# Performance work log

Hardware: AMD Instinct MI355X
Metric: run time of the kernel (lower is better)

Reference implementation:

```python
import jax, jax.numpy as jnp
import numpy as np

B, S, D, H = 128, 512, 256, 256


def _lstm_cell(Wih, Whh, b, x_t, h, c):
    # PyTorch LSTM gate order: i, f, g, o. b = b_ih + b_hh (mathematically equivalent).
    z = x_t @ Wih.T + h @ Whh.T + b  # [B, 4H]
    i, f, g, o = jnp.split(z, 4, axis=-1)
    i = jax.nn.sigmoid(i)
    f = jax.nn.sigmoid(f)
    g = jnp.tanh(g)
    o = jax.nn.sigmoid(o)
    c = f * c + i * g
    h = o * jnp.tanh(c)
    return h, c


def setup_inputs() -> dict:
    key = jax.random.key(0)
    ks = jax.random.split(key, 12)
    s = 1.0 / np.sqrt(H)
    f32 = jnp.float32
    return {
        "x": jax.random.normal(ks[0], (B, S, D), f32),
        "enc_Wih": jax.random.uniform(ks[1], (4 * H, D), f32, -s, s),
        "enc_Whh": jax.random.uniform(ks[2], (4 * H, H), f32, -s, s),
        "enc_b": jax.random.uniform(ks[3], (4 * H,), f32, -s, s),
        "dec_Wih": jax.random.uniform(ks[4], (4 * H, D), f32, -s, s),
        "dec_Whh": jax.random.uniform(ks[5], (4 * H, H), f32, -s, s),
        "dec_b": jax.random.uniform(ks[6], (4 * H,), f32, -s, s),
        "W1_w": jax.random.uniform(ks[7], (H, H), f32, -s, s),
        "W1_b": jax.random.uniform(ks[8], (H,), f32, -s, s),
        "W2_w": jax.random.uniform(ks[9], (H, H), f32, -s, s),
        "W2_b": jax.random.uniform(ks[10], (H,), f32, -s, s),
        "vt_w": jax.random.uniform(ks[11], (H,), f32, -s, s),
    }


def reference(x, enc_Wih, enc_Whh, enc_b, dec_Wih, dec_Whh, dec_b,
              W1_w, W1_b, W2_w, W2_b, vt_w):
    b_, s_, d_ = x.shape
    h0 = jnp.zeros((b_, H), x.dtype)
    c0 = jnp.zeros((b_, H), x.dtype)

    # ---- encoder LSTM over time ----
    def enc_step(carry, x_t):
        h, c = carry
        h, c = _lstm_cell(enc_Wih, enc_Whh, enc_b, x_t, h, c)
        return (h, c), h

    (h, c), enc_out = jax.lax.scan(enc_step, (h0, c0), jnp.swapaxes(x, 0, 1))
    enc_out = jnp.swapaxes(enc_out, 0, 1)  # [B, S, H]

    # W1(encoder_outputs) is loop-invariant; compute once (same math as original)
    enc_proj = enc_out @ W1_w.T + W1_b  # [B, S, H]

    # ---- pointer decode loop ----
    def dec_step(carry, _):
        h, c, din = carry
        h, c = _lstm_cell(dec_Wih, dec_Whh, dec_b, din, h, c)
        q = h @ W2_w.T + W2_b  # [B, H]
        u = jnp.einsum('bsh,h->bs', jnp.tanh(enc_proj + q[:, None, :]), vt_w)
        probs = jax.nn.softmax(u, axis=1)  # [B, S]
        din = jnp.einsum('bs,bsh->bh', probs, enc_out)
        return (h, c, din), probs

    din0 = jnp.zeros((b_, d_), x.dtype)
    _, probs_seq = jax.lax.scan(dec_step, (h, c, din0), None, length=s_)
    return jnp.swapaxes(probs_seq, 0, 1)  # [B, S, S]
```

## Files before the change

### kernel.cpp

```cpp
#include <hip/hip_runtime.h>
#include <hip/hip_fp16.h>

typedef _Float16 h2_t __attribute__((ext_vector_type(2)));
typedef unsigned int u32x4 __attribute__((ext_vector_type(4)));

#define KEXP 2.8853900817779268f

#define BARRIER() do { \
    asm volatile("s_waitcnt lgkmcnt(0)" ::: "memory"); \
    __builtin_amdgcn_s_barrier(); \
    asm volatile("" ::: "memory"); \
} while (0)

__device__ __forceinline__ float fdot2(unsigned int a, unsigned int b, float c) {
#if __has_builtin(__builtin_amdgcn_fdot2)
    return __builtin_amdgcn_fdot2(__builtin_bit_cast(h2_t, a), __builtin_bit_cast(h2_t, b), c, false);
#else
    h2_t ha = __builtin_bit_cast(h2_t, a), hb = __builtin_bit_cast(h2_t, b);
    return c + (float)ha[0]*(float)hb[0] + (float)ha[1]*(float)hb[1];
#endif
}

__device__ __forceinline__ unsigned int pk16(float a, float b) {
    auto h = __builtin_amdgcn_cvt_pkrtz(a, b);
    return __builtin_bit_cast(unsigned int, h);
}

__device__ __forceinline__ float rcp_(float x) {
#if __has_builtin(__builtin_amdgcn_rcpf)
    return __builtin_amdgcn_rcpf(x);
#else
    return 1.0f / x;
#endif
}

__device__ __forceinline__ float sigm(float x) { return rcp_(1.0f + __expf(-x)); }
__device__ __forceinline__ float tanh_(float x) {
    float e = __expf(2.0f * x);
    return 1.0f - 2.0f * rcp_(e + 1.0f);
}

__device__ __forceinline__ unsigned int rcp1p2exp(unsigned int s) {
    __half2 e = h2exp2(__builtin_bit_cast(__half2, s));
    __half2 d = __hadd2(e, __float2half2_rn(1.0f));
    return __builtin_bit_cast(unsigned int, h2rcp(d));
}
__device__ __forceinline__ unsigned int hadd2u(unsigned int a, unsigned int b) {
    return __builtin_bit_cast(unsigned int,
        __hadd2(__builtin_bit_cast(__half2, a), __builtin_bit_cast(__half2, b)));
}

__device__ __forceinline__ void st_u32(unsigned int* p, unsigned int v) {
    __hip_atomic_store(p, v, __ATOMIC_RELAXED, __HIP_MEMORY_SCOPE_AGENT);
}
__device__ __forceinline__ unsigned int ld_u32(const unsigned int* p) {
    return __hip_atomic_load(p, __ATOMIC_RELAXED, __HIP_MEMORY_SCOPE_AGENT);
}
__device__ __forceinline__ float h2f_lo(unsigned int v) {
    return __half2float(__ushort_as_half((unsigned short)(v & 0xffffu)));
}
__device__ __forceinline__ float h2f_hi(unsigned int v) {
    return __half2float(__ushort_as_half((unsigned short)(v >> 16)));
}

__global__ void init_flags_kernel(unsigned int* flags) {
    flags[threadIdx.x * 32] = 0u;
}

__global__ __launch_bounds__(256) void prep_kernel(
    const float* __restrict__ encWhh, const float* __restrict__ decWih,
    const float* __restrict__ decWhh, const float* __restrict__ W2w,
    u32x4* __restrict__ We8, u32x4* __restrict__ Wi8, u32x4* __restrict__ Wh8, u32x4* __restrict__ W28)
{
    int id = blockIdx.x * 256 + threadIdx.x;
    if (id < 3 * 32768) {
        int mat = id >> 15, local = id & 32767;
        int j = local & 1023, k8 = local >> 10;
        const float* src = mat == 0 ? encWhh : (mat == 1 ? decWih : decWhh);
        u32x4* dst = mat == 0 ? We8 : (mat == 1 ? Wi8 : Wh8);
        const float* p = src + (size_t)j * 256 + k8 * 8;
        float4 a = *(const float4*)p; float4 c = *(const float4*)(p + 4);
        u32x4 v; v[0] = pk16(a.x, a.y); v[1] = pk16(a.z, a.w);
        v[2] = pk16(c.x, c.y); v[3] = pk16(c.z, c.w);
        dst[k8 * 1024 + j] = v;
    } else {
        int local = id - 3 * 32768;
        if (local < 8192) {
            int m = local & 255, k8 = local >> 8;
            const float* p = W2w + (size_t)m * 256 + k8 * 8;
            float4 a = *(const float4*)p; float4 c = *(const float4*)(p + 4);
            u32x4 v; v[0] = pk16(a.x, a.y); v[1] = pk16(a.z, a.w);
            v[2] = pk16(c.x, c.y); v[3] = pk16(c.z, c.w);
            W28[k8 * 256 + m] = v;
        }
    }
}

template<int A_IS_F16, int TR_OUT>
__global__ __launch_bounds__(256) void gemm_kernel(
    const void* __restrict__ A_, const float* __restrict__ Bw,
    const float* __restrict__ bias, unsigned short* __restrict__ C, int N, float scale)
{
    __shared__ float As[16][68];
    __shared__ float Bs[16][132];
    const int t = threadIdx.x;
    const int row0 = blockIdx.y * 64, col0 = blockIdx.x * 128;
    const int ty = t >> 4, tx = t & 15;
    const int lm = t & 63, lkq = t >> 6;
    const int ln = t & 127, lkq2 = t >> 7;
    float acc[4][8] = {};
    for (int k0 = 0; k0 < 256; k0 += 16) {
        float4 av;
        if constexpr (A_IS_F16) {
            const unsigned short* A = (const unsigned short*)A_;
            uint2 ha = *(const uint2*)(A + (size_t)(row0 + lm) * 256 + k0 + lkq * 4);
            h2_t h0 = __builtin_bit_cast(h2_t, ha.x);
            h2_t h1 = __builtin_bit_cast(h2_t, ha.y);
            av = make_float4((float)h0[0], (float)h0[1], (float)h1[0], (float)h1[1]);
        } else {
            av = *(const float4*)((const float*)A_ + (size_t)(row0 + lm) * 256 + k0 + lkq * 4);
        }
        const float* bp = Bw + (size_t)(col0 + ln) * 256 + k0 + lkq2 * 8;
        float4 bv0 = *(const float4*)bp;
        float4 bv1 = *(const float4*)(bp + 4);
        __syncthreads();
        As[lkq * 4 + 0][lm] = av.x;
        As[lkq * 4 + 1][lm] = av.y;
        As[lkq * 4 + 2][lm] = av.z;
        As[lkq * 4 + 3][lm] = av.w;
        Bs[lkq2 * 8 + 0][ln] = bv0.x;
        Bs[lkq2 * 8 + 1][ln] = bv0.y;
        Bs[lkq2 * 8 + 2][ln] = bv0.z;
        Bs[lkq2 * 8 + 3][ln] = bv0.w;
        Bs[lkq2 * 8 + 4][ln] = bv1.x;
        Bs[lkq2 * 8 + 5][ln] = bv1.y;
        Bs[lkq2 * 8 + 6][ln] = bv1.z;
        Bs[lkq2 * 8 + 7][ln] = bv1.w;
        __syncthreads();
        #pragma unroll
        for (int kk = 0; kk < 16; ++kk) {
            float4 a = *(float4*)&As[kk][ty * 4];
            float4 b0 = *(float4*)&Bs[kk][tx * 8];
            float4 b1 = *(float4*)&Bs[kk][tx * 8 + 4];
            float ar[4] = {a.x, a.y, a.z, a.w};
            float br[8] = {b0.x, b0.y, b0.z, b0.w, b1.x, b1.y, b1.z, b1.w};
            #pragma unroll
            for (int i = 0; i < 4; ++i)
                #pragma unroll
                for (int j = 0; j < 8; ++j)
                    acc[i][j] = fmaf(ar[i], br[j], acc[i][j]);
        }
    }
    float bv[8];
    #pragma unroll
    for (int j = 0; j < 8; ++j) bv[j] = bias[col0 + tx * 8 + j];
    #pragma unroll
    for (int i = 0; i < 4; ++i) {
        unsigned int w0 = pk16((acc[i][0] + bv[0]) * scale, (acc[i][1] + bv[1]) * scale);
        unsigned int w1 = pk16((acc[i][2] + bv[2]) * scale, (acc[i][3] + bv[3]) * scale);
        unsigned int w2 = pk16((acc[i][4] + bv[4]) * scale, (acc[i][5] + bv[5]) * scale);
        unsigned int w3 = pk16((acc[i][6] + bv[6]) * scale, (acc[i][7] + bv[7]) * scale);
        uint4 val = make_uint4(w0, w1, w2, w3);
        if constexpr (TR_OUT) {
            int rr = row0 + ty * 4 + i;
            int bb = rr >> 9, s = rr & 511;
            int c8 = (col0 >> 3) + tx;
            ((uint4*)C)[(size_t)bb * 16384 + (size_t)c8 * 512 + s] = val;
        } else {
            *(uint4*)(C + (size_t)(row0 + ty * 4 + i) * N + col0 + tx * 8) = val;
        }
    }
}

__global__ __launch_bounds__(1024) void encoder_kernel(
    const unsigned short* __restrict__ Xproj, const u32x4* __restrict__ We8,
    float* __restrict__ hfin, float* __restrict__ cfin,
    unsigned short* __restrict__ enc_h, unsigned int* __restrict__ encT)
{
    const int b = blockIdx.x, t = threadIdx.x;
    __shared__ __align__(16) float zs[1024];
    __shared__ __align__(16) unsigned int hh2[128];
    if (t < 128) hh2[t] = 0u;
    float c_reg = 0.f, hprev = 0.f, hcur = 0.f;
    __syncthreads();
    const unsigned short* xp = Xproj + (size_t)b * 512 * 1024 + t;
    for (int step = 0; step < 512; ++step) {
        float acc = __half2float(__ushort_as_half(__builtin_nontemporal_load(xp)));
        #pragma unroll 8
        for (int k8 = 0; k8 < 32; ++k8) {
            u32x4 wv = We8[k8 * 1024 + t];
            u32x4 hv = *(const u32x4*)&hh2[k8 * 4];
            acc = fdot2(wv[0], hv[0], acc); acc = fdot2(wv[1], hv[1], acc);
            acc = fdot2(wv[2], hv[2], acc); acc = fdot2(wv[3], hv[3], acc);
        }
        zs[t] = acc;
        __syncthreads();
        if (t < 256) {
            float ig = sigm(zs[t]), fg = sigm(zs[t + 256]);
            float gg = tanh_(zs[t + 512]), og = sigm(zs[t + 768]);
            c_reg = fg * c_reg + ig * gg;
            float h = og * tanh_(c_reg);
            float hnb = __shfl_down(h, 1);
            if (!(t & 1)) hh2[t >> 1] = pk16(h, hnb);
            __builtin_nontemporal_store(__half_as_ushort(__float2half_rn(h)),
                                        enc_h + (size_t)(b * 512 + step) * 256 + t);
            if (step & 1) {
                int s2 = step >> 1;
                encT[(size_t)b * 65536 + (size_t)((s2 >> 2) * 256 + t) * 4 + (s2 & 3)] = pk16(hprev, h);
            }
            hprev = h; hcur = h;
        }
        __syncthreads();
        xp += 1024;
    }
    if (t < 256) { hfin[b * 256 + t] = hcur; cfin[b * 256 + t] = c_reg; }
}

__global__ __launch_bounds__(512, 4) void decoder_kernel(
    const u32x4* __restrict__ Wi8, const u32x4* __restrict__ Wh8, const u32x4* __restrict__ W28,
    const float* __restrict__ dec_b, const float* __restrict__ W2b, const float* __restrict__ vtw,
    const float* __restrict__ hfin, const float* __restrict__ cfin,
    const u32x4* __restrict__ projT, const u32x4* __restrict__ encT,
    unsigned int* __restrict__ xgate, unsigned int* __restrict__ xdin,
    unsigned int* __restrict__ xsum, unsigned int* __restrict__ flags,
    float* __restrict__ out)
{
    const int blk = blockIdx.x;
    const int b = blk & 127, g = blk >> 7;
    const int t = threadIdx.x;
    const int lane = t & 63, w = t >> 6;

    __shared__ __align__(16) float zs[512];
    __shared__ __align__(16) unsigned int hh2[128];
    __shared__ __align__(16) unsigned int din2[128];
    __shared__ __align__(16) unsigned int qp2[128];
    __shared__ __align__(16) unsigned int mv2u[128];
    __shared__ __align__(16) unsigned int p2u[64];
    __shared__ float wreds[8];
    __shared__ float svtS, rsS;

    const int q4 = b * 4 + g;
    unsigned int* fl_me = flags + q4 * 32;
    unsigned int* fl_p0 = flags + (b * 4 + ((g + 1) & 3)) * 32;
    unsigned int* fl_p1 = flags + (b * 4 + ((g + 2) & 3)) * 32;
    unsigned int* fl_p2 = flags + (b * 4 + ((g + 3) & 3)) * 32;
    unsigned int* xg_me = xgate + q4 * 128;
    unsigned int* xd_me = xdin + q4 * 256;

    float ca = 0.f, cb = 0.f;
    if (t < 128) {
        ca = cfin[b * 256 + 2 * t];
        cb = cfin[b * 256 + 2 * t + 1];
        din2[t] = 0u;
        mv2u[t] = pk16(-2.f * vtw[2 * t], -2.f * vtw[2 * t + 1]);
    }
    const float bja = (t < 256) ? dec_b[g * 256 + t] : 0.f;
    const float w2b_r = (t < 256) ? W2b[t] : 0.f;
    if (t < 256) zs[t] = vtw[t];
    __syncthreads();
    if (t < 64) {
        float v = zs[t] + zs[t + 64] + zs[t + 128] + zs[t + 192];
        #pragma unroll
        for (int off = 1; off < 64; off <<= 1) v += __shfl_xor(v, off);
        if (t == 0) svtS = v;
    }
    if (t < 256) {
        float h0 = hfin[b * 256 + t];
        float hnb = __shfl_down(h0, 1);
        if (!(t & 1)) hh2[t >> 1] = pk16(h0, hnb);
    }
    __syncthreads();
    const float svt = svtS;

    const int jl = t & 255, kh = t >> 8;
    const u32x4* wp = (kh ? Wh8 : Wi8) + (g * 256 + jl);
    const unsigned int* vls = kh ? (const unsigned int*)hh2 : (const unsigned int*)din2;
    const int mC = t & 255, sc = t >> 8;
    const int sl4 = t >> 2, qr = t & 3;
    const int s_g = g * 128 + sl4;
    const u32x4* pD = projT + (size_t)b * 16384 + (size_t)(qr * 8) * 512 + s_g;
    const u32x4* fD = encT + (size_t)b * 16384 + (size_t)(g * 16 + sc * 8) * 256 + mC;
    float* outp = out + (size_t)b * 262144;

    for (int step = 0; step < 512; ++step) {
        float acc = 0.f;
        #pragma unroll 8
        for (int k8 = 0; k8 < 32; ++k8) {
            u32x4 wv = wp[k8 * 1024];
            u32x4 hv = *(const u32x4*)&vls[k8 * 4];
            acc = fdot2(wv[0], hv[0], acc); acc = fdot2(wv[1], hv[1], acc);
            acc = fdot2(wv[2], hv[2], acc); acc = fdot2(wv[3], hv[3], acc);
        }
        zs[t] = acc;
        BARRIER();
        if (t < 256) {
            float z = bja + zs[t] + zs[t + 256];
            float gv = (g == 2) ? tanh_(z) : sigm(z);
            float gnx = __shfl_down(gv, 1);
            if (!(t & 1))
                st_u32(&xg_me[t >> 1],
                       (unsigned int)__half_as_ushort(__float2half_rn(gv)) |
                       ((unsigned int)__half_as_ushort(__float2half_rn(gnx)) << 16));
        }
        asm volatile("s_waitcnt vmcnt(0)" ::: "memory");
        BARRIER();
        if (t == 0) {
            unsigned int T = (unsigned)(2 * step + 1);
            st_u32(fl_me, T);
            for (;;) {
                unsigned int f0 = ld_u32(fl_p0), f1 = ld_u32(fl_p1), f2 = ld_u32(fl_p2);
                if (f0 >= T && f1 >= T && f2 >= T) break;
                __builtin_amdgcn_s_sleep(1);
            }
        }
        BARRIER();
        if (t < 128) {
            unsigned int G0 = ld_u32(&xgate[(b * 4 + 0) * 128 + t]);
            unsigned int G1 = ld_u32(&xgate[(b * 4 + 1) * 128 + t]);
            unsigned int G2 = ld_u32(&xgate[(b * 4 + 2) * 128 + t]);
            unsigned int G3 = ld_u32(&xgate[(b * 4 + 3) * 128 + t]);
            ca = h2f_lo(G1) * ca + h2f_lo(G0) * h2f_lo(G2);
            cb = h2f_hi(G1) * cb + h2f_hi(G0) * h2f_hi(G2);
            float ha = h2f_lo(G3) * tanh_(ca);
            float hb = h2f_hi(G3) * tanh_(cb);
            hh2[t] = pk16(ha, hb);
        }
        BARRIER();
        {
            float qa = 0.f;
            #pragma unroll
            for (int i = 0; i < 16; ++i) {
                int k8 = sc * 16 + i;
                u32x4 wv = W28[k8 * 256 + mC];
                u32x4 hv = *(const u32x4*)&hh2[k8 * 4];
                qa = fdot2(wv[0], hv[0], qa); qa = fdot2(wv[1], hv[1], qa);
                qa = fdot2(wv[2], hv[2], qa); qa = fdot2(wv[3], hv[3], qa);
            }
            zs[t] = qa;
        }
        BARRIER();
        if (t < 256) {
            float q = (w2b_r + zs[t] + zs[t + 256]) * KEXP;
            float qnx = __shfl_down(q, 1);
            if (!(t & 1)) qp2[t >> 1] = pk16(q, qnx);
        }
        BARRIER();
        float e;
        u32x4 fv[8];
        {
            float up = 0.f;
            #pragma unroll 4
            for (int i = 0; i < 8; ++i) {
                u32x4 pv = pD[i * 512];
                int c = qr * 8 + i;
                u32x4 qh = *(const u32x4*)&qp2[c * 4];
                u32x4 mv = *(const u32x4*)&mv2u[c * 4];
                up = fdot2(mv[0], rcp1p2exp(hadd2u(pv[0], qh[0])), up);
                up = fdot2(mv[1], rcp1p2exp(hadd2u(pv[1], qh[1])), up);
                up = fdot2(mv[2], rcp1p2exp(hadd2u(pv[2], qh[2])), up);
                up = fdot2(mv[3], rcp1p2exp(hadd2u(pv[3], qh[3])), up);
            }
            up += __shfl_xor(up, 1);
            up += __shfl_xor(up, 2);
            e = __expf(up + svt);
            #pragma unroll
            for (int j = 0; j < 8; ++j) fv[j] = fD[j * 256];
            float enx = __shfl_down(e, 4);
            if (!(t & 7)) p2u[t >> 3] = pk16(e, enx);
            float ws = e;
            #pragma unroll
            for (int off = 1; off < 64; off <<= 1) ws += __shfl_xor(ws, off);
            if (lane == 0) wreds[w] = ws;
        }
        BARRIER();
        {
            float fa = 0.f;
            #pragma unroll
            for (int j = 0; j < 8; ++j) {
                u32x4 ev = fv[j];
                u32x4 pw = *(const u32x4*)&p2u[(sc * 8 + j) * 4];
                fa = fdot2(ev[0], pw[0], fa); fa = fdot2(ev[1], pw[1], fa);
                fa = fdot2(ev[2], pw[2], fa); fa = fdot2(ev[3], pw[3], fa);
            }
            zs[t] = fa;
        }
        BARRIER();
        float dpart = 0.f;
        if (t < 256) {
            dpart = zs[t] + zs[t + 256];
            st_u32(&xd_me[t], __builtin_bit_cast(unsigned int, dpart));
        }
        if (t == 0) {
            float ls = 0.f;
            #pragma unroll
            for (int k = 0; k < 8; ++k) ls += wreds[k];
            st_u32(&xsum[q4 * 32], __builtin_bit_cast(unsigned int, ls * 0.25f));
        }
        asm volatile("s_waitcnt vmcnt(0)" ::: "memory");
        BARRIER();
        if (t == 0) {
            unsigned int T = (unsigned)(2 * step + 2);
            st_u32(fl_me, T);
            for (;;) {
                unsigned int f0 = ld_u32(fl_p0), f1 = ld_u32(fl_p1), f2 = ld_u32(fl_p2);
                if (f0 >= T && f1 >= T && f2 >= T) break;
                __builtin_amdgcn_s_sleep(1);
            }
            float gs = __builtin_bit_cast(float, ld_u32(&xsum[(b * 4 + 0) * 32]))
                     + __builtin_bit_cast(float, ld_u32(&xsum[(b * 4 + 1) * 32]))
                     + __builtin_bit_cast(float, ld_u32(&xsum[(b * 4 + 2) * 32]))
                     + __builtin_bit_cast(float, ld_u32(&xsum[(b * 4 + 3) * 32]));
            rsS = rcp_(gs);
        }
        BARRIER();
        {
            float rs = rsS;
            if (t < 256) {
                float dsum = dpart;
                #pragma unroll
                for (int dg = 1; dg < 4; ++dg) {
                    int gp = (g + dg) & 3;
                    dsum += __builtin_bit_cast(float, ld_u32(&xdin[(b * 4 + gp) * 256 + t]));
                }
                float dval = dsum * rs;
                float dnx = __shfl_down(dval, 1);
                if (!(t & 1)) din2[t >> 1] = pk16(dval, dnx);
            }
            if ((t & 3) == 0)
                outp[(size_t)step * 512 + s_g] = e * rs;
        }
        BARRIER();
    }
}

extern "C" void kernel_launch(void* const* d_in, const int* in_sizes, int n_in,
                              void* d_out, int out_size, void* d_ws, size_t ws_size,
                              hipStream_t stream) {
    const float* x      = (const float*)d_in[0];
    const float* encWih = (const float*)d_in[1];
    const float* encWhh = (const float*)d_in[2];
    const float* enc_b  = (const float*)d_in[3];
    const float* decWih = (const float*)d_in[4];
    const float* decWhh = (const float*)d_in[5];
    const float* dec_bp = (const float*)d_in[6];
    const float* W1w    = (const float*)d_in[7];
    const float* W1b    = (const float*)d_in[8];
    const float* W2w    = (const float*)d_in[9];
    const float* W2bp   = (const float*)d_in[10];
    const float* vtw    = (const float*)d_in[11];

    char* ws = (char*)d_ws;
    u32x4* We8 = (u32x4*)(ws);
    u32x4* Wi8 = (u32x4*)(ws + 524288);
    u32x4* Wh8 = (u32x4*)(ws + 1048576);
    u32x4* W28 = (u32x4*)(ws + 1572864);
    unsigned short* enc_h = (unsigned short*)(ws + 1703936);
    unsigned int*   encT  = (unsigned int*)(ws + 35258368);
    unsigned short* projT = (unsigned short*)(ws + 68812800);
    float* hfin = (float*)(ws + 102367232);
    float* cfin = (float*)(ws + 102498304);

    unsigned int* flags = (unsigned int*)(ws + 1703936);
    unsigned int* xsum  = (unsigned int*)(ws + 1703936 + 65536);
    unsigned int* xgate = (unsigned int*)(ws + 1703936 + 131072);
    unsigned int* xdin  = (unsigned int*)(ws + 1703936 + 131072 + 262144);

    unsigned short* Xproj = (unsigned short*)d_out;

    prep_kernel<<<416, 256, 0, stream>>>(encWhh, decWih, decWhh, W2w, We8, Wi8, Wh8, W28);
    gemm_kernel<0, 0><<<dim3(8, 1024), 256, 0, stream>>>(x, encWih, enc_b, Xproj, 1024, 1.0f);
    encoder_kernel<<<128, 1024, 0, stream>>>(Xproj, We8, hfin, cfin, enc_h, (unsigned int*)encT);
    gemm_kernel<1, 1><<<dim3(2, 1024), 256, 0, stream>>>(enc_h, W1w, W1b, projT, 256, KEXP);
    init_flags_kernel<<<1, 512, 0, stream>>>(flags);
    decoder_kernel<<<512, 512, 0, stream>>>(Wi8, Wh8, W28, dec_bp, W2bp, vtw,
                                            hfin, cfin, (const u32x4*)projT, (const u32x4*)encT,
                                            xgate, xdin, xsum, flags, (float*)d_out);
}
```

Measured before the change: 16.86 ms.

## Batch four sequences per decoder block with register-resident LSTM weights

The decoder now processes four batch elements per workgroup (128 blocks instead of 512). Each thread keeps its slice of the input and recurrent LSTM weights in registers for the whole run, so these weights are no longer re-read from memory every step, and one weight fetch serves four dot products. The cost is much higher register pressure (launch bounds drop to 2 waves/EU), fewer blocks to spread across CUs, and four times more serial per-block work in the attention and softmax phases. Cross-block flag synchronization is now shared by four batches at once.

```diff
diff --git a/kernel.cpp b/kernel.cpp
--- a/kernel.cpp
+++ b/kernel.cpp
@@ -21,6 +21,12 @@
 #endif
 }
 
+__device__ __forceinline__ float dot4(u32x4 a, u32x4 b, float c) {
+    c = fdot2(a[0], b[0], c); c = fdot2(a[1], b[1], c);
+    c = fdot2(a[2], b[2], c); c = fdot2(a[3], b[3], c);
+    return c;
+}
+
 __device__ __forceinline__ unsigned int pk16(float a, float b) {
     auto h = __builtin_amdgcn_cvt_pkrtz(a, b);
     return __builtin_bit_cast(unsigned int, h);
@@ -55,6 +61,9 @@
 }
 __device__ __forceinline__ unsigned int ld_u32(const unsigned int* p) {
     return __hip_atomic_load(p, __ATOMIC_RELAXED, __HIP_MEMORY_SCOPE_AGENT);
+}
+__device__ __forceinline__ float ld_f32(const unsigned int* p) {
+    return __builtin_bit_cast(float, ld_u32(p));
 }
 __device__ __forceinline__ float h2f_lo(unsigned int v) {
     return __half2float(__ushort_as_half((unsigned short)(v & 0xffffu)));
@@ -190,8 +199,7 @@
         for (int k8 = 0; k8 < 32; ++k8) {
             u32x4 wv = We8[k8 * 1024 + t];
             u32x4 hv = *(const u32x4*)&hh2[k8 * 4];
-            acc = fdot2(wv[0], hv[0], acc); acc = fdot2(wv[1], hv[1], acc);
-            acc = fdot2(wv[2], hv[2], acc); acc = fdot2(wv[3], hv[3], acc);
+            acc = dot4(wv, hv, acc);
         }
         zs[t] = acc;
         __syncthreads();
@@ -216,7 +224,7 @@
     if (t < 256) { hfin[b * 256 + t] = hcur; cfin[b * 256 + t] = c_reg; }
 }
 
-__global__ __launch_bounds__(512, 4) void decoder_kernel(
+__global__ __launch_bounds__(512, 2) void decoder_kernel(
     const u32x4* __restrict__ Wi8, const u32x4* __restrict__ Wh8, const u32x4* __restrict__ W28,
     const float* __restrict__ dec_b, const float* __restrict__ W2b, const float* __restrict__ vtw,
     const float* __restrict__ hfin, const float* __restrict__ cfin,
@@ -226,81 +234,108 @@
     float* __restrict__ out)
 {
     const int blk = blockIdx.x;
-    const int b = blk & 127, g = blk >> 7;
+    const int gr = blk & 31, g = blk >> 5;
     const int t = threadIdx.x;
     const int lane = t & 63, w = t >> 6;
-
-    __shared__ __align__(16) float zs[512];
-    __shared__ __align__(16) unsigned int hh2[128];
-    __shared__ __align__(16) unsigned int din2[128];
-    __shared__ __align__(16) unsigned int qp2[128];
+    const int bbase = gr * 4;
+
+    __shared__ float zsp[4][512];
+    __shared__ __align__(16) unsigned int hh2[4][128];
+    __shared__ __align__(16) unsigned int din2[4][128];
+    __shared__ __align__(16) unsigned int qp2[4][128];
     __shared__ __align__(16) unsigned int mv2u[128];
-    __shared__ __align__(16) unsigned int p2u[64];
-    __shared__ float wreds[8];
-    __shared__ float svtS, rsS;
-
-    const int q4 = b * 4 + g;
-    unsigned int* fl_me = flags + q4 * 32;
-    unsigned int* fl_p0 = flags + (b * 4 + ((g + 1) & 3)) * 32;
-    unsigned int* fl_p1 = flags + (b * 4 + ((g + 2) & 3)) * 32;
-    unsigned int* fl_p2 = flags + (b * 4 + ((g + 3) & 3)) * 32;
-    unsigned int* xg_me = xgate + q4 * 128;
-    unsigned int* xd_me = xdin + q4 * 256;
-
-    float ca = 0.f, cb = 0.f;
+    __shared__ __align__(16) unsigned int p2u[4][64];
+    __shared__ float wreds[8][4];
+    __shared__ float svtS, rsS[4];
+
+    const int r = t & 255, kh = t >> 8;
+    u32x4 wih[16], whh[16];
+    #pragma unroll
+    for (int i = 0; i < 16; ++i) wih[i] = Wi8[(size_t)(kh * 16 + i) * 1024 + g * 256 + r];
+    #pragma unroll
+    for (int i = 0; i < 16; ++i) whh[i] = Wh8[(size_t)(kh * 16 + i) * 1024 + g * 256 + r];
+
+    float cA[4], cB[4];
+    #pragma unroll
+    for (int b = 0; b < 4; ++b) { cA[b] = 0.f; cB[b] = 0.f; }
     if (t < 128) {
-        ca = cfin[b * 256 + 2 * t];
-        cb = cfin[b * 256 + 2 * t + 1];
-        din2[t] = 0u;
+        #pragma unroll
+        for (int b = 0; b < 4; ++b) {
+            cA[b] = cfin[(bbase + b) * 256 + 2 * t];
+            cB[b] = cfin[(bbase + b) * 256 + 2 * t + 1];
+            din2[b][t] = 0u;
+        }
         mv2u[t] = pk16(-2.f * vtw[2 * t], -2.f * vtw[2 * t + 1]);
     }
     const float bja = (t < 256) ? dec_b[g * 256 + t] : 0.f;
     const float w2b_r = (t < 256) ? W2b[t] : 0.f;
-    if (t < 256) zs[t] = vtw[t];
+    if (t < 256) zsp[0][t] = vtw[t];
     __syncthreads();
     if (t < 64) {
-        float v = zs[t] + zs[t + 64] + zs[t + 128] + zs[t + 192];
+        float v = zsp[0][t] + zsp[0][t + 64] + zsp[0][t + 128] + zsp[0][t + 192];
         #pragma unroll
         for (int off = 1; off < 64; off <<= 1) v += __shfl_xor(v, off);
         if (t == 0) svtS = v;
     }
     if (t < 256) {
-        float h0 = hfin[b * 256 + t];
-        float hnb = __shfl_down(h0, 1);
-        if (!(t & 1)) hh2[t >> 1] = pk16(h0, hnb);
+        #pragma unroll
+        for (int b = 0; b < 4; ++b) {
+            float h0 = hfin[(bbase + b) * 256 + t];
+            float h0n = __shfl_down(h0, 1);
+            if (!(t & 1)) hh2[b][t >> 1] = pk16(h0, h0n);
+        }
     }
     __syncthreads();
     const float svt = svtS;
 
-    const int jl = t & 255, kh = t >> 8;
-    const u32x4* wp = (kh ? Wh8 : Wi8) + (g * 256 + jl);
-    const unsigned int* vls = kh ? (const unsigned int*)hh2 : (const unsigned int*)din2;
-    const int mC = t & 255, sc = t >> 8;
-    const int sl4 = t >> 2, qr = t & 3;
-    const int s_g = g * 128 + sl4;
-    const u32x4* pD = projT + (size_t)b * 16384 + (size_t)(qr * 8) * 512 + s_g;
-    const u32x4* fD = encT + (size_t)b * 16384 + (size_t)(g * 16 + sc * 8) * 256 + mC;
-    float* outp = out + (size_t)b * 262144;
+    const int q4 = gr * 4 + g;
+    unsigned int* fl_me = flags + q4 * 32;
+    unsigned int* fl_p0 = flags + (gr * 4 + ((g + 1) & 3)) * 32;
+    unsigned int* fl_p1 = flags + (gr * 4 + ((g + 2) & 3)) * 32;
+    unsigned int* fl_p2 = flags + (gr * 4 + ((g + 3) & 3)) * 32;
+    unsigned int* xg_me = xgate + q4 * 512;
+    unsigned int* xd_me = xdin + q4 * 1024;
+
+    const int sl = t >> 2, qr = t & 3;
+    const int hF = t & 255, scF = t >> 8;
+    const size_t pDoff = (size_t)(qr * 8) * 512 + g * 128 + sl;
+    const size_t fDoff = (size_t)(g * 16 + scF * 8) * 256 + hF;
 
     for (int step = 0; step < 512; ++step) {
-        float acc = 0.f;
-        #pragma unroll 8
-        for (int k8 = 0; k8 < 32; ++k8) {
-            u32x4 wv = wp[k8 * 1024];
-            u32x4 hv = *(const u32x4*)&vls[k8 * 4];
-            acc = fdot2(wv[0], hv[0], acc); acc = fdot2(wv[1], hv[1], acc);
-            acc = fdot2(wv[2], hv[2], acc); acc = fdot2(wv[3], hv[3], acc);
-        }
-        zs[t] = acc;
+        {
+            float a0 = 0.f, a1 = 0.f, a2 = 0.f, a3 = 0.f;
+            #pragma unroll
+            for (int i = 0; i < 16; ++i) {
+                u32x4 wv = wih[i];
+                u32x4 d0 = *(const u32x4*)&din2[0][kh * 64 + i * 4];
+                u32x4 d1 = *(const u32x4*)&din2[1][kh * 64 + i * 4];
+                u32x4 d2 = *(const u32x4*)&din2[2][kh * 64 + i * 4];
+                u32x4 d3 = *(const u32x4*)&din2[3][kh * 64 + i * 4];
+                a0 = dot4(wv, d0, a0); a1 = dot4(wv, d1, a1);
+                a2 = dot4(wv, d2, a2); a3 = dot4(wv, d3, a3);
+            }
+            #pragma unroll
+            for (int i = 0; i < 16; ++i) {
+                u32x4 wv = whh[i];
+                u32x4 h0 = *(const u32x4*)&hh2[0][kh * 64 + i * 4];
+                u32x4 h1 = *(const u32x4*)&hh2[1][kh * 64 + i * 4];
+                u32x4 h2 = *(const u32x4*)&hh2[2][kh * 64 + i * 4];
+                u32x4 h3 = *(const u32x4*)&hh2[3][kh * 64 + i * 4];
+                a0 = dot4(wv, h0, a0); a1 = dot4(wv, h1, a1);
+                a2 = dot4(wv, h2, a2); a3 = dot4(wv, h3, a3);
+            }
+            zsp[0][t] = a0; zsp[1][t] = a1; zsp[2][t] = a2; zsp[3][t] = a3;
+        }
         BARRIER();
         if (t < 256) {
-            float z = bja + zs[t] + zs[t + 256];
-            float gv = (g == 2) ? tanh_(z) : sigm(z);
-            float gnx = __shfl_down(gv, 1);
-            if (!(t & 1))
-                st_u32(&xg_me[t >> 1],
-                       (unsigned int)__half_as_ushort(__float2half_rn(gv)) |
-                       ((unsigned int)__half_as_ushort(__float2half_rn(gnx)) << 16));
+            float gv[4];
+            #pragma unroll
+            for (int b = 0; b < 4; ++b) {
+                float z = bja + zsp[b][t] + zsp[b][t + 256];
+                gv[b] = (g == 2) ? tanh_(z) : sigm(z);
+            }
+            st_u32(&xg_me[t], pk16(gv[0], gv[1]));
+            st_u32(&xg_me[256 + t], pk16(gv[2], gv[3]));
         }
         asm volatile("s_waitcnt vmcnt(0)" ::: "memory");
         BARRIER();
@@ -315,86 +350,116 @@
         }
         BARRIER();
         if (t < 128) {
-            unsigned int G0 = ld_u32(&xgate[(b * 4 + 0) * 128 + t]);
-            unsigned int G1 = ld_u32(&xgate[(b * 4 + 1) * 128 + t]);
-            unsigned int G2 = ld_u32(&xgate[(b * 4 + 2) * 128 + t]);
-            unsigned int G3 = ld_u32(&xgate[(b * 4 + 3) * 128 + t]);
-            ca = h2f_lo(G1) * ca + h2f_lo(G0) * h2f_lo(G2);
-            cb = h2f_hi(G1) * cb + h2f_hi(G0) * h2f_hi(G2);
-            float ha = h2f_lo(G3) * tanh_(ca);
-            float hb = h2f_hi(G3) * tanh_(cb);
-            hh2[t] = pk16(ha, hb);
+            #pragma unroll
+            for (int bp = 0; bp < 2; ++bp) {
+                unsigned int Xi_a = ld_u32(&xgate[(gr * 4 + 0) * 512 + bp * 256 + 2 * t]);
+                unsigned int Xi_b = ld_u32(&xgate[(gr * 4 + 0) * 512 + bp * 256 + 2 * t + 1]);
+                unsigned int Xf_a = ld_u32(&xgate[(gr * 4 + 1) * 512 + bp * 256 + 2 * t]);
+                unsigned int Xf_b = ld_u32(&xgate[(gr * 4 + 1) * 512 + bp * 256 + 2 * t + 1]);
+                unsigned int Xg_a = ld_u32(&xgate[(gr * 4 + 2) * 512 + bp * 256 + 2 * t]);
+                unsigned int Xg_b = ld_u32(&xgate[(gr * 4 + 2) * 512 + bp * 256 + 2 * t + 1]);
+                unsigned int Xo_a = ld_u32(&xgate[(gr * 4 + 3) * 512 + bp * 256 + 2 * t]);
+                unsigned int Xo_b = ld_u32(&xgate[(gr * 4 + 3) * 512 + bp * 256 + 2 * t + 1]);
+                int b0i = bp * 2, b1i = bp * 2 + 1;
+                cA[b0i] = h2f_lo(Xf_a) * cA[b0i] + h2f_lo(Xi_a) * h2f_lo(Xg_a);
+                cB[b0i] = h2f_lo(Xf_b) * cB[b0i] + h2f_lo(Xi_b) * h2f_lo(Xg_b);
+                hh2[b0i][t] = pk16(h2f_lo(Xo_a) * tanh_(cA[b0i]), h2f_lo(Xo_b) * tanh_(cB[b0i]));
+                cA[b1i] = h2f_hi(Xf_a) * cA[b1i] + h2f_hi(Xi_a) * h2f_hi(Xg_a);
+                cB[b1i] = h2f_hi(Xf_b) * cB[b1i] + h2f_hi(Xi_b) * h2f_hi(Xg_b);
+                hh2[b1i][t] = pk16(h2f_hi(Xo_a) * tanh_(cA[b1i]), h2f_hi(Xo_b) * tanh_(cB[b1i]));
+            }
         }
         BARRIER();
         {
-            float qa = 0.f;
-            #pragma unroll
+            float q0 = 0.f, q1 = 0.f, q2 = 0.f, q3 = 0.f;
+            #pragma unroll 4
             for (int i = 0; i < 16; ++i) {
-                int k8 = sc * 16 + i;
-                u32x4 wv = W28[k8 * 256 + mC];
-                u32x4 hv = *(const u32x4*)&hh2[k8 * 4];
-                qa = fdot2(wv[0], hv[0], qa); qa = fdot2(wv[1], hv[1], qa);
-                qa = fdot2(wv[2], hv[2], qa); qa = fdot2(wv[3], hv[3], qa);
-            }
-            zs[t] = qa;
+                int k8 = kh * 16 + i;
+                u32x4 wv = W28[k8 * 256 + r];
+                u32x4 h0 = *(const u32x4*)&hh2[0][k8 * 4];
+                u32x4 h1 = *(const u32x4*)&hh2[1][k8 * 4];
+                u32x4 h2 = *(const u32x4*)&hh2[2][k8 * 4];
+                u32x4 h3 = *(const u32x4*)&hh2[3][k8 * 4];
+                q0 = dot4(wv, h0, q0); q1 = dot4(wv, h1, q1);
+                q2 = dot4(wv, h2, q2); q3 = dot4(wv, h3, q3);
+            }
+            zsp[0][t] = q0; zsp[1][t] = q1; zsp[2][t] = q2; zsp[3][t] = q3;
         }
         BARRIER();
         if (t < 256) {
-            float q = (w2b_r + zs[t] + zs[t + 256]) * KEXP;
-            float qnx = __shfl_down(q, 1);
-            if (!(t & 1)) qp2[t >> 1] = pk16(q, qnx);
-        }
-        BARRIER();
-        float e;
-        u32x4 fv[8];
+            #pragma unroll
+            for (int b = 0; b < 4; ++b) {
+                float q = (w2b_r + zsp[b][t] + zsp[b][t + 256]) * KEXP;
+                float qn = __shfl_down(q, 1);
+                if (!(t & 1)) qp2[b][t >> 1] = pk16(q, qn);
+            }
+        }
+        BARRIER();
+        float eb[4];
         {
-            float up = 0.f;
-            #pragma unroll 4
-            for (int i = 0; i < 8; ++i) {
-                u32x4 pv = pD[i * 512];
-                int c = qr * 8 + i;
-                u32x4 qh = *(const u32x4*)&qp2[c * 4];
-                u32x4 mv = *(const u32x4*)&mv2u[c * 4];
-                up = fdot2(mv[0], rcp1p2exp(hadd2u(pv[0], qh[0])), up);
-                up = fdot2(mv[1], rcp1p2exp(hadd2u(pv[1], qh[1])), up);
-                up = fdot2(mv[2], rcp1p2exp(hadd2u(pv[2], qh[2])), up);
-                up = fdot2(mv[3], rcp1p2exp(hadd2u(pv[3], qh[3])), up);
-            }
-            up += __shfl_xor(up, 1);
-            up += __shfl_xor(up, 2);
-            e = __expf(up + svt);
-            #pragma unroll
-            for (int j = 0; j < 8; ++j) fv[j] = fD[j * 256];
-            float enx = __shfl_down(e, 4);
-            if (!(t & 7)) p2u[t >> 3] = pk16(e, enx);
-            float ws = e;
-            #pragma unroll
-            for (int off = 1; off < 64; off <<= 1) ws += __shfl_xor(ws, off);
-            if (lane == 0) wreds[w] = ws;
+            #pragma unroll
+            for (int b = 0; b < 4; ++b) {
+                const u32x4* pD = projT + (size_t)(bbase + b) * 16384 + pDoff;
+                u32x4 pv[8];
+                #pragma unroll
+                for (int i = 0; i < 8; ++i) pv[i] = pD[i * 512];
+                float u = 0.f;
+                #pragma unroll
+                for (int i = 0; i < 8; ++i) {
+                    int c = qr * 8 + i;
+                    u32x4 qh = *(const u32x4*)&qp2[b][c * 4];
+                    u32x4 mv = *(const u32x4*)&mv2u[c * 4];
+                    u = fdot2(mv[0], rcp1p2exp(hadd2u(pv[i][0], qh[0])), u);
+                    u = fdot2(mv[1], rcp1p2exp(hadd2u(pv[i][1], qh[1])), u);
+                    u = fdot2(mv[2], rcp1p2exp(hadd2u(pv[i][2], qh[2])), u);
+                    u = fdot2(mv[3], rcp1p2exp(hadd2u(pv[i][3], qh[3])), u);
+                }
+                u += __shfl_xor(u, 1);
+                u += __shfl_xor(u, 2);
+                float e = __expf(u + svt);
+                eb[b] = e;
+                float en = __shfl_down(e, 4);
+                if (!(t & 7)) p2u[b][t >> 3] = pk16(e, en);
+                float ws = e;
+                #pragma unroll
+                for (int off = 1; off < 64; off <<= 1) ws += __shfl_xor(ws, off);
+                if (lane == 0) wreds[w][b] = ws;
+            }
         }
         BARRIER();
         {
-            float fa = 0.f;
-            #pragma unroll
-            for (int j = 0; j < 8; ++j) {
-                u32x4 ev = fv[j];
-                u32x4 pw = *(const u32x4*)&p2u[(sc * 8 + j) * 4];
-                fa = fdot2(ev[0], pw[0], fa); fa = fdot2(ev[1], pw[1], fa);
-                fa = fdot2(ev[2], pw[2], fa); fa = fdot2(ev[3], pw[3], fa);
-            }
-            zs[t] = fa;
-        }
-        BARRIER();
-        float dpart = 0.f;
+            #pragma unroll
+            for (int b = 0; b < 4; ++b) {
+                const u32x4* fD = encT + (size_t)(bbase + b) * 16384 + fDoff;
+                u32x4 fv[8];
+                #pragma unroll
+                for (int j = 0; j < 8; ++j) fv[j] = fD[j * 256];
+                float fa = 0.f;
+                #pragma unroll
+                for (int j = 0; j < 8; ++j) {
+                    u32x4 pw = *(const u32x4*)&p2u[b][(scF * 8 + j) * 4];
+                    fa = dot4(fv[j], pw, fa);
+                }
+                zsp[b][t] = fa;
+            }
+        }
+        BARRIER();
+        float dp[4] = {0.f, 0.f, 0.f, 0.f};
         if (t < 256) {
-            dpart = zs[t] + zs[t + 256];
-            st_u32(&xd_me[t], __builtin_bit_cast(unsigned int, dpart));
+            #pragma unroll
+            for (int b = 0; b < 4; ++b) {
+                dp[b] = zsp[b][t] + zsp[b][t + 256];
+                st_u32(&xd_me[b * 256 + t], __builtin_bit_cast(unsigned int, dp[b]));
+            }
         }
         if (t == 0) {
-            float ls = 0.f;
-            #pragma unroll
-            for (int k = 0; k < 8; ++k) ls += wreds[k];
-            st_u32(&xsum[q4 * 32], __builtin_bit_cast(unsigned int, ls * 0.25f));
+            #pragma unroll
+            for (int b = 0; b < 4; ++b) {
+                float s = 0.f;
+                #pragma unroll
+                for (int k = 0; k < 8; ++k) s += wreds[k][b];
+                st_u32(&xsum[q4 * 32 + b], __builtin_bit_cast(unsigned int, s * 0.25f));
+            }
         }
         asm volatile("s_waitcnt vmcnt(0)" ::: "memory");
         BARRIER();
@@ -406,28 +471,35 @@
                 if (f0 >= T && f1 >= T && f2 >= T) break;
                 __builtin_amdgcn_s_sleep(1);
             }
-            float gs = __builtin_bit_cast(float, ld_u32(&xsum[(b * 4 + 0) * 32]))
-                     + __builtin_bit_cast(float, ld_u32(&xsum[(b * 4 + 1) * 32]))
-                     + __builtin_bit_cast(float, ld_u32(&xsum[(b * 4 + 2) * 32]))
-                     + __builtin_bit_cast(float, ld_u32(&xsum[(b * 4 + 3) * 32]));
-            rsS = rcp_(gs);
+            #pragma unroll
+            for (int b = 0; b < 4; ++b) {
+                float gs = 0.f;
+                #pragma unroll
+                for (int gp = 0; gp < 4; ++gp) gs += ld_f32(&xsum[(gr * 4 + gp) * 32 + b]);
+                rsS[b] = rcp_(gs);
+            }
         }
         BARRIER();
         {
-            float rs = rsS;
             if (t < 256) {
-                float dsum = dpart;
-                #pragma unroll
-                for (int dg = 1; dg < 4; ++dg) {
-                    int gp = (g + dg) & 3;
-                    dsum += __builtin_bit_cast(float, ld_u32(&xdin[(b * 4 + gp) * 256 + t]));
+                #pragma unroll
+                for (int b = 0; b < 4; ++b) {
+                    float d = dp[b];
+                    #pragma unroll
+                    for (int dg = 1; dg < 4; ++dg) {
+                        int gp = (g + dg) & 3;
+                        d += ld_f32(&xdin[(gr * 4 + gp) * 1024 + b * 256 + t]);
+                    }
+                    float dv = d * rsS[b];
+                    float dvn = __shfl_down(dv, 1);
+                    if (!(t & 1)) din2[b][t >> 1] = pk16(dv, dvn);
                 }
-                float dval = dsum * rs;
-                float dnx = __shfl_down(dval, 1);
-                if (!(t & 1)) din2[t >> 1] = pk16(dval, dnx);
-            }
-            if ((t & 3) == 0)
-                outp[(size_t)step * 512 + s_g] = e * rs;
+            }
+            if (!(t & 3)) {
+                #pragma unroll
+                for (int b = 0; b < 4; ++b)
+                    out[(size_t)(bbase + b) * 262144 + (size_t)step * 512 + g * 128 + sl] = eb[b] * rsS[b];
+            }
         }
         BARRIER();
     }
@@ -461,9 +533,9 @@
     float* cfin = (float*)(ws + 102498304);
 
     unsigned int* flags = (unsigned int*)(ws + 1703936);
-    unsigned int* xsum  = (unsigned int*)(ws + 1703936 + 65536);
-    unsigned int* xgate = (unsigned int*)(ws + 1703936 + 131072);
-    unsigned int* xdin  = (unsigned int*)(ws + 1703936 + 131072 + 262144);
+    unsigned int* xsum  = (unsigned int*)(ws + 1703936 + 32768);
+    unsigned int* xgate = (unsigned int*)(ws + 1703936 + 65536);
+    unsigned int* xdin  = (unsigned int*)(ws + 1703936 + 65536 + 262144);
 
     unsigned short* Xproj = (unsigned short*)d_out;
 
@@ -471,8 +543,8 @@
     gemm_kernel<0, 0><<<dim3(8, 1024), 256, 0, stream>>>(x, encWih, enc_b, Xproj, 1024, 1.0f);
     encoder_kernel<<<128, 1024, 0, stream>>>(Xproj, We8, hfin, cfin, enc_h, (unsigned int*)encT);
     gemm_kernel<1, 1><<<dim3(2, 1024), 256, 0, stream>>>(enc_h, W1w, W1b, projT, 256, KEXP);
-    init_flags_kernel<<<1, 512, 0, stream>>>(flags);
-    decoder_kernel<<<512, 512, 0, stream>>>(Wi8, Wh8, W28, dec_bp, W2bp, vtw,
+    init_flags_kernel<<<1, 128, 0, stream>>>(flags);
+    decoder_kernel<<<128, 512, 0, stream>>>(Wi8, Wh8, W28, dec_bp, W2bp, vtw,
                                             hfin, cfin, (const u32x4*)projT, (const u32x4*)encT,
                                             xgate, xdin, xsum, flags, (float*)d_out);
 }
```

After: 25.18 ms. +49.4%, slower.
